# Optimization experiments

Hardware: AMD Instinct MI355X
Metric: run time of the kernel (lower is better)

The kernel has to match this reference:

```python
import jax, jax.numpy as jnp
import numpy as np

B, D_MODEL, HIDEEN, HEAD, IMG_H, IMG_W = 16, 512, 512, 8, 32, 32
D_K = D_MODEL // HEAD
EPS = 1e-5


def setup_inputs() -> dict:
    key = jax.random.key(0)
    ks = jax.random.split(key, 9)
    s_in = 1.0 / np.sqrt(D_MODEL)
    s_h = 1.0 / np.sqrt(HIDEEN)
    return {
        "x": jax.random.normal(ks[0], (B, D_MODEL, IMG_H, IMG_W), jnp.float32),
        "Wq": jax.random.uniform(ks[1], (HIDEEN, D_MODEL), jnp.float32, -s_in, s_in),
        "bq": jax.random.uniform(ks[2], (HIDEEN,), jnp.float32, -s_in, s_in),
        "Wk": jax.random.uniform(ks[3], (HIDEEN, D_MODEL), jnp.float32, -s_in, s_in),
        "bk": jax.random.uniform(ks[4], (HIDEEN,), jnp.float32, -s_in, s_in),
        "Wv": jax.random.uniform(ks[5], (HIDEEN, D_MODEL), jnp.float32, -s_in, s_in),
        "bv": jax.random.uniform(ks[6], (HIDEEN,), jnp.float32, -s_in, s_in),
        "Wo": jax.random.uniform(ks[7], (HIDEEN, HIDEEN), jnp.float32, -s_h, s_h),
        "bo": jax.random.uniform(ks[8], (HIDEEN,), jnp.float32, -s_h, s_h),
    }


def _conv1x1(x, W, b):
    # x: [B, Cin, H, W], W: [Cout, Cin]
    return jnp.einsum("bchw,oc->bohw", x, W) + b[None, :, None, None]


def _heads(t):
    # torch: [B, C, H, W] -> view(B, -1, head, d_k) -> transpose(1, 2)
    return t.reshape(B, -1, HEAD, D_K).transpose(0, 2, 1, 3)  # [B, head, N, d_k]


def reference(x, Wq, bq, Wk, bk, Wv, bv, Wo, bo):
    q = _heads(_conv1x1(x, Wq, bq))
    k = _heads(_conv1x1(x, Wk, bk))
    v = _heads(_conv1x1(x, Wv, bv))
    scores = jnp.einsum("bhnd,bhmd->bhnm", q, k) / np.sqrt(D_K).astype(np.float32)
    attn = jax.nn.softmax(scores, axis=-1)
    out = jnp.einsum("bhnm,bhmd->bhnd", attn, v)  # [B, head, N, d_k]
    # back to image layout: [B, N, head*d_k] -> [B, hideen, H, W]
    out = out.transpose(0, 2, 1, 3).reshape(B, -1, HEAD * D_K)
    out = out.transpose(0, 2, 1).reshape(B, -1, IMG_H, IMG_W)
    out = _conv1x1(out, Wo, bo)
    # InstanceNorm2d (affine=False, biased var, eps=1e-5)
    mu = out.mean(axis=(2, 3), keepdims=True)
    var = out.var(axis=(2, 3), keepdims=True)
    out = (out - mu) / jnp.sqrt(var + EPS)
    # original applies the SAME attn_out conv a second time
    out = _conv1x1(out, Wo, bo)
    return out
```

## Files before the change

### kernel.cpp

```cpp
#include <hip/hip_runtime.h>


typedef short bf16x8_t __attribute__((ext_vector_type(8)));
typedef float f32x4_t  __attribute__((ext_vector_type(4)));

union U4 {
  uint4 u;
  bf16x8_t v;
  unsigned short us[8];
};

__device__ __forceinline__ unsigned short f2bf(float f) {
  union { float f; unsigned int u; } x; x.f = f;
  unsigned int r = x.u + 0x7fffu + ((x.u >> 16) & 1u);
  return (unsigned short)(r >> 16);
}

#define BATCH_STRIDE (512 * 1024)

__global__ __launch_bounds__(256) void cvtx_k(
    const float* __restrict__ x, unsigned short* __restrict__ xb)
{
  __shared__ float tile[32][33];
  const int b = blockIdx.z, c0 = blockIdx.y * 32, n0 = blockIdx.x * 32;
  const int t = threadIdx.x;
  {
    const int cl_ = t >> 3, n4 = (t & 7) * 4;
    const float4 u = *(const float4*)(x + (size_t)b * BATCH_STRIDE
                                      + (size_t)(c0 + cl_) * 1024 + n0 + n4);
    tile[cl_][n4] = u.x; tile[cl_][n4 + 1] = u.y;
    tile[cl_][n4 + 2] = u.z; tile[cl_][n4 + 3] = u.w;
  }
  __syncthreads();
  {
    const int nl = t >> 3, c4 = (t & 7) * 4;
    ushort4 o;
    o.x = f2bf(tile[c4][nl]);     o.y = f2bf(tile[c4 + 1][nl]);
    o.z = f2bf(tile[c4 + 2][nl]); o.w = f2bf(tile[c4 + 3][nl]);
    *(ushort4*)(xb + (size_t)b * BATCH_STRIDE + (size_t)(n0 + nl) * 512
                + c0 + c4) = o;
  }
}

template<int OUTF>
__device__ __forceinline__ void gemm_core(
    const float* __restrict__ W, const float* __restrict__ bias,
    const unsigned short* __restrict__ src, void* __restrict__ dst,
    int m0, int n0, int b, unsigned short* sA, unsigned short* sB)
{
  const int t = threadIdx.x;
  const int lane = t & 63, wv = t >> 6, qd = lane >> 4, cl = lane & 15;
  const int wm = wv >> 1, wn = wv & 1;
  const unsigned short* srcb = src + (size_t)b * BATCH_STRIDE + (size_t)n0 * 512;

  f32x4_t acc[4][4];
  #pragma unroll
  for (int i = 0; i < 4; ++i)
    #pragma unroll
    for (int f = 0; f < 4; ++f) acc[i][f] = (f32x4_t){0.f, 0.f, 0.f, 0.f};

  const int ar = t >> 2, akf = (t & 3) * 8;

  for (int kk = 0; kk < 512; kk += 32) {
    if (kk) __syncthreads();
    #pragma unroll
    for (int p = 0; p < 2; ++p) {
      const int row = p * 64 + ar;
      const float* wr = W + (size_t)(m0 + row) * 512 + kk + akf;
      const float4 w0 = *(const float4*)wr;
      const float4 w1 = *(const float4*)(wr + 4);
      U4 wa;
      wa.us[0] = f2bf(w0.x); wa.us[1] = f2bf(w0.y);
      wa.us[2] = f2bf(w0.z); wa.us[3] = f2bf(w0.w);
      wa.us[4] = f2bf(w1.x); wa.us[5] = f2bf(w1.y);
      wa.us[6] = f2bf(w1.z); wa.us[7] = f2bf(w1.w);
      *(uint4*)(sA + row * 40 + akf) = wa.u;
      *(uint4*)(sB + row * 40 + akf) =
          *(const uint4*)(srcb + (size_t)row * 512 + kk + akf);
    }
    __syncthreads();
    U4 af[4], bf[4];
    #pragma unroll
    for (int i = 0; i < 4; ++i) {
      af[i].u = *(const uint4*)(sA + (wm * 64 + i * 16 + cl) * 40 + qd * 8);
      bf[i].u = *(const uint4*)(sB + (wn * 64 + i * 16 + cl) * 40 + qd * 8);
    }
    #pragma unroll
    for (int i = 0; i < 4; ++i)
      #pragma unroll
      for (int f = 0; f < 4; ++f)
        acc[i][f] = __builtin_amdgcn_mfma_f32_16x16x32_bf16(
            af[i].v, bf[f].v, acc[i][f], 0, 0, 0);
  }

  #pragma unroll
  for (int i = 0; i < 4; ++i) {
    #pragma unroll
    for (int r = 0; r < 4; ++r) {
      const int o = m0 + wm * 64 + i * 16 + qd * 4 + r;
      const float bv = bias[o];
      #pragma unroll
      for (int f = 0; f < 4; ++f) {
        const int n = n0 + wn * 64 + f * 16 + cl;
        const size_t idx = (size_t)b * BATCH_STRIDE + (size_t)o * 1024 + n;
        const float val = acc[i][f][r] + bv;
        if (OUTF) ((float*)dst)[idx] = val;
        else      ((unsigned short*)dst)[idx] = f2bf(val);
      }
    }
  }
}

struct QKVArgs {
  const float* W[3];
  const float* bias[3];
  unsigned short* dst[3];
};

__global__ __launch_bounds__(256) void qkv_k(
    QKVArgs args, const unsigned short* __restrict__ xb)
{
  __shared__ __align__(16) unsigned short sA[128 * 40];
  __shared__ __align__(16) unsigned short sB[128 * 40];
  const int widx = blockIdx.y >> 2;
  const int m0 = (blockIdx.y & 3) * 128;
  gemm_core<0>(args.W[widx], args.bias[widx], xb, args.dst[widx],
               m0, blockIdx.x * 128, blockIdx.z, sA, sB);
}

template<int OUTF>
__global__ __launch_bounds__(256) void gemm_wo_k(
    const float* __restrict__ W, const float* __restrict__ bias,
    const unsigned short* __restrict__ src, void* __restrict__ dst)
{
  __shared__ __align__(16) unsigned short sA[128 * 40];
  __shared__ __align__(16) unsigned short sB[128 * 40];
  gemm_core<OUTF>(W, bias, src, dst, blockIdx.y * 128, blockIdx.x * 128,
                  blockIdx.z, sA, sB);
}

__global__ __launch_bounds__(256) void vt_k(
    const unsigned short* __restrict__ src, unsigned short* __restrict__ dst)
{
  __shared__ unsigned short tile[32][36];
  const int b = blockIdx.z, j0 = blockIdx.y * 32, p0 = blockIdx.x * 32;
  const int t = threadIdx.x;
  {
    const int pr = t >> 3, jc = (t & 7) * 4;
    *(ushort4*)&tile[pr][jc] = *(const ushort4*)(
        src + (size_t)b * BATCH_STRIDE + (size_t)(p0 + pr) * 512 + j0 + jc);
  }
  __syncthreads();
  {
    const int jr = t >> 3, pc = (t & 7) * 4;
    ushort4 o;
    o.x = tile[pc][jr];     o.y = tile[pc + 1][jr];
    o.z = tile[pc + 2][jr]; o.w = tile[pc + 3][jr];
    *(ushort4*)(dst + (size_t)b * BATCH_STRIDE + (size_t)(j0 + jr) * 1024
                + p0 + pc) = o;
  }
}

__global__ __launch_bounds__(256) void attn_k(
    const unsigned short* __restrict__ Q,
    const unsigned short* __restrict__ K,
    const unsigned short* __restrict__ Vt,
    unsigned short* __restrict__ O)
{
  __shared__ __align__(16) unsigned short sK[64 * 72];
  __shared__ __align__(16) unsigned short sV[64 * 72];
  __shared__ __align__(16) unsigned short sP[4 * 16 * 72];

  const int t = threadIdx.x;
  const int lane = t & 63, wv = t >> 6, qd = lane >> 4, cl = lane & 15;

  const int g = blockIdx.y * 16 + blockIdx.x;
  const int xcd = g & 7, rest = g >> 3;
  const int iblk = rest & 15;
  const int bh = (rest >> 4) * 8 + xcd;
  const int b = bh >> 3, h = bh & 7;
  const int i0 = iblk * 64;
  const size_t bbase = (size_t)b * BATCH_STRIDE;
  const int hoff = h * 64;

  U4 aq0, aq1;
  {
    const unsigned short* qp =
        Q + bbase + (size_t)(i0 + wv * 16 + cl) * 512 + hoff + qd * 8;
    aq0.u = *(const uint4*)qp;
    aq1.u = *(const uint4*)(qp + 32);
  }

  f32x4_t oacc[4];
  #pragma unroll
  for (int f = 0; f < 4; ++f) oacc[f] = (f32x4_t){0.f, 0.f, 0.f, 0.f};
  float rs[4] = {0.f, 0.f, 0.f, 0.f};

  for (int j0 = 0; j0 < 1024; j0 += 64) {
    __syncthreads();
    #pragma unroll
    for (int p = 0; p < 2; ++p) {
      const int row = p * 32 + (t >> 3), c8 = (t & 7) * 8;
      *(uint4*)(sK + row * 72 + c8) =
          *(const uint4*)(K + bbase + (size_t)(j0 + row) * 512 + hoff + c8);
      *(uint4*)(sV + row * 72 + c8) =
          *(const uint4*)(Vt + bbase + (size_t)(hoff + row) * 1024 + j0 + c8);
    }
    __syncthreads();

    f32x4_t s[4];
    #pragma unroll
    for (int nh = 0; nh < 4; ++nh) {
      s[nh] = (f32x4_t){0.f, 0.f, 0.f, 0.f};
      U4 bk0; bk0.u = *(const uint4*)(sK + (nh * 16 + cl) * 72 + qd * 8);
      U4 bk1; bk1.u = *(const uint4*)(sK + (nh * 16 + cl) * 72 + 32 + qd * 8);
      s[nh] = __builtin_amdgcn_mfma_f32_16x16x32_bf16(aq0.v, bk0.v, s[nh], 0, 0, 0);
      s[nh] = __builtin_amdgcn_mfma_f32_16x16x32_bf16(aq1.v, bk1.v, s[nh], 0, 0, 0);
    }

    #pragma unroll
    for (int nh = 0; nh < 4; ++nh) {
      #pragma unroll
      for (int r = 0; r < 4; ++r) {
        const float pv = __expf(s[nh][r] * 0.125f);
        sP[wv * 1152 + (qd * 4 + r) * 72 + nh * 16 + cl] = f2bf(pv);
        rs[r] += pv;
      }
    }

    __syncthreads();

    U4 pf0, pf1;
    pf0.u = *(const uint4*)(sP + wv * 1152 + cl * 72 + qd * 8);
    pf1.u = *(const uint4*)(sP + wv * 1152 + cl * 72 + 32 + qd * 8);
    #pragma unroll
    for (int f = 0; f < 4; ++f) {
      U4 vf0, vf1;
      vf0.u = *(const uint4*)(sV + (f * 16 + cl) * 72 + qd * 8);
      vf1.u = *(const uint4*)(sV + (f * 16 + cl) * 72 + 32 + qd * 8);
      oacc[f] = __builtin_amdgcn_mfma_f32_16x16x32_bf16(pf0.v, vf0.v, oacc[f], 0, 0, 0);
      oacc[f] = __builtin_amdgcn_mfma_f32_16x16x32_bf16(pf1.v, vf1.v, oacc[f], 0, 0, 0);
    }
  }

  #pragma unroll
  for (int m = 1; m < 16; m <<= 1)
    #pragma unroll
    for (int r = 0; r < 4; ++r) rs[r] += __shfl_xor(rs[r], m);

  #pragma unroll
  for (int f = 0; f < 4; ++f) {
    #pragma unroll
    for (int r = 0; r < 4; ++r) {
      const int i = i0 + wv * 16 + qd * 4 + r;
      const int j = hoff + f * 16 + cl;
      O[bbase + (size_t)i * 512 + j] = f2bf(oacc[f][r] / rs[r]);
    }
  }
}

__global__ __launch_bounds__(256) void norm_k(
    const float* __restrict__ x, unsigned short* __restrict__ y)
{
  __shared__ float tile[8][1028];
  __shared__ float shm[8], shv[8];
  const int b = blockIdx.x >> 6, c0 = (blockIdx.x & 63) * 8;
  const int t = threadIdx.x;
  const int ch = t >> 5, ln = t & 31;
  const float* xr = x + (size_t)b * BATCH_STRIDE + (size_t)(c0 + ch) * 1024;
  float s1 = 0.f, s2 = 0.f;
  #pragma unroll
  for (int j = 0; j < 8; ++j) {
    const int n = ln * 4 + j * 128;
    const float4 u = *(const float4*)(xr + n);
    tile[ch][n] = u.x; tile[ch][n + 1] = u.y;
    tile[ch][n + 2] = u.z; tile[ch][n + 3] = u.w;
    s1 += u.x + u.y + u.z + u.w;
    s2 += u.x * u.x + u.y * u.y + u.z * u.z + u.w * u.w;
  }
  #pragma unroll
  for (int m = 1; m < 32; m <<= 1) {
    s1 += __shfl_xor(s1, m);
    s2 += __shfl_xor(s2, m);
  }
  if (ln == 0) {
    const float mean = s1 * (1.f / 1024.f);
    const float var = s2 * (1.f / 1024.f) - mean * mean;
    shm[ch] = mean;
    shv[ch] = rsqrtf(var + 1e-5f);
  }
  __syncthreads();
  unsigned short* yb = y + (size_t)b * BATCH_STRIDE;
  #pragma unroll
  for (int jn = 0; jn < 4; ++jn) {
    const int n = t + jn * 256;
    U4 o;
    #pragma unroll
    for (int c = 0; c < 8; ++c)
      o.us[c] = f2bf((tile[c][n] - shm[c]) * shv[c]);
    *(uint4*)(yb + (size_t)n * 512 + c0) = o.u;
  }
}

extern "C" void kernel_launch(void* const* d_in, const int* in_sizes, int n_in,
                              void* d_out, int out_size, void* d_ws, size_t ws_size,
                              hipStream_t stream) {
  const float* x  = (const float*)d_in[0];
  const float* Wq = (const float*)d_in[1];
  const float* bq = (const float*)d_in[2];
  const float* Wk = (const float*)d_in[3];
  const float* bk = (const float*)d_in[4];
  const float* Wv = (const float*)d_in[5];
  const float* bv = (const float*)d_in[6];
  const float* Wo = (const float*)d_in[7];
  const float* bo = (const float*)d_in[8];

  const size_t BUF = (size_t)16 * BATCH_STRIDE;
  unsigned short* xb = (unsigned short*)d_ws;
  unsigned short* Qb = xb + BUF;
  unsigned short* Kb = Qb + BUF;
  unsigned short* Vb = (unsigned short*)d_out;
  unsigned short* Ob = Vb + BUF;
  unsigned short* Vt = xb;
  float*          out1f = (float*)d_ws;
  unsigned short* out1n = Kb;

  QKVArgs qa;
  qa.W[0] = Wq; qa.W[1] = Wk; qa.W[2] = Wv;
  qa.bias[0] = bq; qa.bias[1] = bk; qa.bias[2] = bv;
  qa.dst[0] = Qb; qa.dst[1] = Kb; qa.dst[2] = Vb;

  cvtx_k<<<dim3(32, 16, 16), 256, 0, stream>>>(x, xb);
  qkv_k<<<dim3(8, 12, 16), 256, 0, stream>>>(qa, xb);
  vt_k<<<dim3(32, 16, 16), 256, 0, stream>>>(Vb, Vt);
  attn_k<<<dim3(16, 128), 256, 0, stream>>>(Qb, Kb, Vt, Ob);
  gemm_wo_k<1><<<dim3(8, 4, 16), 256, 0, stream>>>(Wo, bo, Ob, out1f);
  norm_k<<<dim3(16 * 64), 256, 0, stream>>>(out1f, out1n);
  gemm_wo_k<1><<<dim3(8, 4, 16), 256, 0, stream>>>(Wo, bo, out1n, d_out);
}
```

Before: 278.9 us.

## Pre-convert weights to bf16 and stage GEMM tiles via global_load_lds

Adds a small kernel that converts Wq/Wk/Wv/Wo to bf16 once per call into scratch buffers, so the GEMM cores no longer reload and convert fp32 weights in every block. The GEMM tile loads now use direct global-to-LDS 16-byte loads instead of going through registers, with the padded LDS stride of 40 removed to fit that layout. The unpadded LDS layout may bring back bank conflicts on the fragment reads, and the extra conversion launches add a little overhead. Scratch buffers are reused carefully so the converted weights sit in regions that are free at that point.

```diff
diff --git a/kernel.cpp b/kernel.cpp
--- a/kernel.cpp
+++ b/kernel.cpp
@@ -14,6 +14,15 @@
   union { float f; unsigned int u; } x; x.f = f;
   unsigned int r = x.u + 0x7fffu + ((x.u >> 16) & 1u);
   return (unsigned short)(r >> 16);
+}
+
+#define AS1 __attribute__((address_space(1)))
+#define AS3 __attribute__((address_space(3)))
+
+__device__ __forceinline__ void gload16(const unsigned short* g,
+                                        unsigned short* l) {
+  __builtin_amdgcn_global_load_lds((const AS1 unsigned int*)g,
+                                   (AS3 unsigned int*)l, 16, 0, 0);
 }
 
 #define BATCH_STRIDE (512 * 1024)
@@ -42,9 +51,25 @@
   }
 }
 
+__global__ __launch_bounds__(256) void cvtw_k(
+    const float* __restrict__ s0, const float* __restrict__ s1,
+    const float* __restrict__ s2, unsigned short* __restrict__ dst)
+{
+  const float* s = (blockIdx.y == 0) ? s0 : (blockIdx.y == 1) ? s1 : s2;
+  const int i = (blockIdx.x * 256 + threadIdx.x) * 8;
+  const float4 a = *(const float4*)(s + i);
+  const float4 c = *(const float4*)(s + i + 4);
+  U4 o;
+  o.us[0] = f2bf(a.x); o.us[1] = f2bf(a.y);
+  o.us[2] = f2bf(a.z); o.us[3] = f2bf(a.w);
+  o.us[4] = f2bf(c.x); o.us[5] = f2bf(c.y);
+  o.us[6] = f2bf(c.z); o.us[7] = f2bf(c.w);
+  *(uint4*)(dst + (size_t)blockIdx.y * 262144 + i) = o.u;
+}
+
 template<int OUTF>
 __device__ __forceinline__ void gemm_core(
-    const float* __restrict__ W, const float* __restrict__ bias,
+    const unsigned short* __restrict__ Wb, const float* __restrict__ bias,
     const unsigned short* __restrict__ src, void* __restrict__ dst,
     int m0, int n0, int b, unsigned short* sA, unsigned short* sB)
 {
@@ -52,38 +77,30 @@
   const int lane = t & 63, wv = t >> 6, qd = lane >> 4, cl = lane & 15;
   const int wm = wv >> 1, wn = wv & 1;
   const unsigned short* srcb = src + (size_t)b * BATCH_STRIDE + (size_t)n0 * 512;
+  const unsigned short* wrow = Wb + (size_t)m0 * 512;
+
+  const int lr = lane >> 2, ls = (lane & 3) * 8;
+  const int r0 = wv * 32;
 
   f32x4_t acc[4][4];
   #pragma unroll
   for (int i = 0; i < 4; ++i)
     #pragma unroll
     for (int f = 0; f < 4; ++f) acc[i][f] = (f32x4_t){0.f, 0.f, 0.f, 0.f};
-
-  const int ar = t >> 2, akf = (t & 3) * 8;
 
   for (int kk = 0; kk < 512; kk += 32) {
     if (kk) __syncthreads();
-    #pragma unroll
-    for (int p = 0; p < 2; ++p) {
-      const int row = p * 64 + ar;
-      const float* wr = W + (size_t)(m0 + row) * 512 + kk + akf;
-      const float4 w0 = *(const float4*)wr;
-      const float4 w1 = *(const float4*)(wr + 4);
-      U4 wa;
-      wa.us[0] = f2bf(w0.x); wa.us[1] = f2bf(w0.y);
-      wa.us[2] = f2bf(w0.z); wa.us[3] = f2bf(w0.w);
-      wa.us[4] = f2bf(w1.x); wa.us[5] = f2bf(w1.y);
-      wa.us[6] = f2bf(w1.z); wa.us[7] = f2bf(w1.w);
-      *(uint4*)(sA + row * 40 + akf) = wa.u;
-      *(uint4*)(sB + row * 40 + akf) =
-          *(const uint4*)(srcb + (size_t)row * 512 + kk + akf);
-    }
+    gload16(wrow + (size_t)(r0 + lr) * 512 + kk + ls,      sA + r0 * 32);
+    gload16(wrow + (size_t)(r0 + 16 + lr) * 512 + kk + ls, sA + (r0 + 16) * 32);
+    gload16(srcb + (size_t)(r0 + lr) * 512 + kk + ls,      sB + r0 * 32);
+    gload16(srcb + (size_t)(r0 + 16 + lr) * 512 + kk + ls, sB + (r0 + 16) * 32);
     __syncthreads();
+
     U4 af[4], bf[4];
     #pragma unroll
     for (int i = 0; i < 4; ++i) {
-      af[i].u = *(const uint4*)(sA + (wm * 64 + i * 16 + cl) * 40 + qd * 8);
-      bf[i].u = *(const uint4*)(sB + (wn * 64 + i * 16 + cl) * 40 + qd * 8);
+      af[i].u = *(const uint4*)(sA + (wm * 64 + i * 16 + cl) * 32 + qd * 8);
+      bf[i].u = *(const uint4*)(sB + (wn * 64 + i * 16 + cl) * 32 + qd * 8);
     }
     #pragma unroll
     for (int i = 0; i < 4; ++i)
@@ -112,7 +129,7 @@
 }
 
 struct QKVArgs {
-  const float* W[3];
+  const unsigned short* W[3];
   const float* bias[3];
   unsigned short* dst[3];
 };
@@ -120,8 +137,8 @@
 __global__ __launch_bounds__(256) void qkv_k(
     QKVArgs args, const unsigned short* __restrict__ xb)
 {
-  __shared__ __align__(16) unsigned short sA[128 * 40];
-  __shared__ __align__(16) unsigned short sB[128 * 40];
+  __shared__ __align__(16) unsigned short sA[128 * 32];
+  __shared__ __align__(16) unsigned short sB[128 * 32];
   const int widx = blockIdx.y >> 2;
   const int m0 = (blockIdx.y & 3) * 128;
   gemm_core<0>(args.W[widx], args.bias[widx], xb, args.dst[widx],
@@ -130,12 +147,12 @@
 
 template<int OUTF>
 __global__ __launch_bounds__(256) void gemm_wo_k(
-    const float* __restrict__ W, const float* __restrict__ bias,
+    const unsigned short* __restrict__ Wb, const float* __restrict__ bias,
     const unsigned short* __restrict__ src, void* __restrict__ dst)
 {
-  __shared__ __align__(16) unsigned short sA[128 * 40];
-  __shared__ __align__(16) unsigned short sB[128 * 40];
-  gemm_core<OUTF>(W, bias, src, dst, blockIdx.y * 128, blockIdx.x * 128,
+  __shared__ __align__(16) unsigned short sA[128 * 32];
+  __shared__ __align__(16) unsigned short sB[128 * 32];
+  gemm_core<OUTF>(Wb, bias, src, dst, blockIdx.y * 128, blockIdx.x * 128,
                   blockIdx.z, sA, sB);
 }
 
@@ -325,16 +342,23 @@
   float*          out1f = (float*)d_ws;
   unsigned short* out1n = Kb;
 
+  unsigned short* Wbf3 = Ob;
+  unsigned short* WoA  = Vb;
+  unsigned short* WoB  = xb;
+
   QKVArgs qa;
-  qa.W[0] = Wq; qa.W[1] = Wk; qa.W[2] = Wv;
+  qa.W[0] = Wbf3; qa.W[1] = Wbf3 + 262144; qa.W[2] = Wbf3 + 524288;
   qa.bias[0] = bq; qa.bias[1] = bk; qa.bias[2] = bv;
   qa.dst[0] = Qb; qa.dst[1] = Kb; qa.dst[2] = Vb;
 
   cvtx_k<<<dim3(32, 16, 16), 256, 0, stream>>>(x, xb);
+  cvtw_k<<<dim3(128, 3), 256, 0, stream>>>(Wq, Wk, Wv, Wbf3);
   qkv_k<<<dim3(8, 12, 16), 256, 0, stream>>>(qa, xb);
   vt_k<<<dim3(32, 16, 16), 256, 0, stream>>>(Vb, Vt);
+  cvtw_k<<<dim3(128, 1), 256, 0, stream>>>(Wo, Wo, Wo, WoA);
   attn_k<<<dim3(16, 128), 256, 0, stream>>>(Qb, Kb, Vt, Ob);
-  gemm_wo_k<1><<<dim3(8, 4, 16), 256, 0, stream>>>(Wo, bo, Ob, out1f);
+  gemm_wo_k<1><<<dim3(8, 4, 16), 256, 0, stream>>>(WoA, bo, Ob, out1f);
   norm_k<<<dim3(16 * 64), 256, 0, stream>>>(out1f, out1n);
-  gemm_wo_k<1><<<dim3(8, 4, 16), 256, 0, stream>>>(Wo, bo, out1n, d_out);
-}
+  cvtw_k<<<dim3(128, 1), 256, 0, stream>>>(Wo, Wo, Wo, WoB);
+  gemm_wo_k<1><<<dim3(8, 4, 16), 256, 0, stream>>>(WoB, bo, out1n, d_out);
+}
```

Measured after the change: 268.2 us. 1.04x faster.
